# Optimization experiments

Hardware: AMD Instinct MI355X
Metric: run time of the kernel (lower is better)

Reference implementation:

```python
import jax, jax.numpy as jnp
import numpy as np

N_EXPERT = 8
TOP_K = 2
NEG_INF = -1e9  # finite sentinel so softmax grads stay well-defined


def setup_inputs() -> dict:
    key = jax.random.key(0)
    ks = jax.random.split(key, 8)
    B, S, D, F, E = 2, 2048, 1024, 4096, N_EXPERT
    sd = 1.0 / np.sqrt(D)
    sf = 1.0 / np.sqrt(F)
    return {
        "x": jax.random.normal(ks[0], (B, S, D), jnp.float32),
        "noise": jax.random.normal(ks[1], (B, S, E), jnp.float32),
        "Wr": jax.random.normal(ks[2], (D, E), jnp.float32) * sd,
        "br": jnp.zeros((E,), jnp.float32),
        "Wn": jax.random.normal(ks[3], (D, E), jnp.float32) * sd,
        "bn": jnp.zeros((E,), jnp.float32),
        "W1": jax.random.normal(ks[4], (E, D, F), jnp.float32) * sd,
        "b1": jnp.zeros((E, F), jnp.float32),
        "W2": jax.random.normal(ks[5], (E, F, D), jnp.float32) * sf,
        "b2": jnp.zeros((E, D), jnp.float32),
    }


def reference(x, noise, Wr, br, Wn, bn, W1, b1, W2, b2):
    # NoisyTopkRouter: logits + noise * softplus(noise_logits)
    logits = jnp.einsum("bsd,de->bse", x, Wr) + br
    noise_logits = jnp.einsum("bsd,de->bse", x, Wn) + bn
    noisy = logits + noise * jax.nn.softplus(noise_logits)

    # keep only top-k logits, -inf elsewhere, softmax over experts
    _, top_ids = jax.lax.top_k(noisy, TOP_K)                  # [B,S,K]
    sel = jnp.sum(jax.nn.one_hot(top_ids, N_EXPERT, dtype=noisy.dtype), axis=-2) > 0  # [B,S,E]
    gates = jax.nn.softmax(jnp.where(sel, noisy, NEG_INF), axis=-1)  # zeros off top-k

    # Expert MLP: Linear -> ReLU -> Linear (dropout = 0 at inference).
    # Gates are exactly zero for non-selected experts, so the dense einsum
    # combine equals the original masked gather/scatter-add.
    h = jax.nn.relu(jnp.einsum("bsd,edf->ebsf", x, W1) + b1[:, None, None, :])
    eo = jnp.einsum("ebsf,efd->ebsd", h, W2) + b2[:, None, None, :]
    return jnp.einsum("bse,ebsd->bsd", gates, eo)
```

## Files before the change

### kernel.cpp

```cpp
#include <hip/hip_runtime.h>

#define T_TOK 4096
#define DDIM 1024
#define FDIM 4096
#define NE 8
#define NPAIR 8192
#define MAXT128 72
#define MAXT256 48

typedef short bf16x8 __attribute__((ext_vector_type(8)));
typedef float f32x4 __attribute__((ext_vector_type(4)));

__device__ inline unsigned short f2bf(float f) {
  union { float f; unsigned u; } a; a.f = f;
  unsigned r = a.u + 0x7fffu + ((a.u >> 16) & 1u);
  return (unsigned short)(r >> 16);
}

__device__ inline float bf2f(ushort u) {
  union { unsigned u; float f; } a; a.u = ((unsigned)u) << 16;
  return a.f;
}

__device__ __forceinline__ void gload16(const void* g, void* l) {
  __builtin_amdgcn_global_load_lds(
      (const __attribute__((address_space(1))) unsigned int*)g,
      (__attribute__((address_space(3))) unsigned int*)l, 16, 0, 0);
}

__global__ __launch_bounds__(256) void router_kernel(
    const float* __restrict__ x, const float* __restrict__ noise,
    const float* __restrict__ Wr, const float* __restrict__ br,
    const float* __restrict__ Wn, const float* __restrict__ bn,
    int* __restrict__ tok_top, float* __restrict__ tok_gate,
    ushort* __restrict__ xb)
{
  int t = blockIdx.x * 4 + (threadIdx.x >> 6);
  int lane = threadIdx.x & 63;
  const float* xr = x + (size_t)t * DDIM;
  ushort* xo = xb + (size_t)t * DDIM;
  float accR[NE] = {}, accN[NE] = {};
  for (int d = lane; d < DDIM; d += 64) {
    float xv = xr[d];
    xo[d] = f2bf(xv);
    const float* wr = Wr + (size_t)d * NE;
    const float* wn = Wn + (size_t)d * NE;
#pragma unroll
    for (int e = 0; e < NE; ++e) {
      accR[e] = fmaf(xv, wr[e], accR[e]);
      accN[e] = fmaf(xv, wn[e], accN[e]);
    }
  }
#pragma unroll
  for (int off = 32; off > 0; off >>= 1) {
#pragma unroll
    for (int e = 0; e < NE; ++e) {
      accR[e] += __shfl_xor(accR[e], off);
      accN[e] += __shfl_xor(accN[e], off);
    }
  }
  if (lane == 0) {
    float noisy[NE];
#pragma unroll
    for (int e = 0; e < NE; ++e) {
      float lg = accR[e] + br[e];
      float nl = accN[e] + bn[e];
      float sp = fmaxf(nl, 0.f) + log1pf(expf(-fabsf(nl)));
      noisy[e] = lg + noise[(size_t)t * NE + e] * sp;
    }
    int e0 = 0;
#pragma unroll
    for (int e = 1; e < NE; ++e) if (noisy[e] > noisy[e0]) e0 = e;
    int e1 = (e0 == 0) ? 1 : 0;
#pragma unroll
    for (int e = 0; e < NE; ++e)
      if (e != e0 && e != e1 && noisy[e] > noisy[e1]) e1 = e;
    float v0 = noisy[e0], v1 = noisy[e1];
    float ex = __expf(v1 - v0);
    float inv = 1.f / (1.f + ex);
    tok_top[t * 2] = e0; tok_top[t * 2 + 1] = e1;
    tok_gate[t * 2] = inv; tok_gate[t * 2 + 1] = ex * inv;
  }
}

__global__ __launch_bounds__(256) void scan_scatter_kernel(
    const int* __restrict__ tok_top, int* __restrict__ off,
    int* __restrict__ tiles128, int* __restrict__ tiles256,
    int* __restrict__ pair_tok, int* __restrict__ tok_ppos)
{
  __shared__ int smat[NE][256];
  __shared__ int tot[NE];
  __shared__ int loff[NE];
  int tid = threadIdx.x;
  int c[NE] = {};
  for (int i = 0; i < 16; ++i) {
    int t = tid * 16 + i;
    int e0 = tok_top[2 * t], e1 = tok_top[2 * t + 1];
#pragma unroll
    for (int e = 0; e < NE; ++e) c[e] += (e0 == e) + (e1 == e);
  }
#pragma unroll
  for (int e = 0; e < NE; ++e) smat[e][tid] = c[e];
  __syncthreads();
  {
    int ge = tid >> 5;
    int gl = tid & 31;
    int vals[8], s = 0;
#pragma unroll
    for (int j = 0; j < 8; ++j) { vals[j] = smat[ge][gl * 8 + j]; s += vals[j]; }
    int incl = s;
#pragma unroll
    for (int d = 1; d < 32; d <<= 1) {
      int o = __shfl_up(incl, d);
      if (gl >= d) incl += o;
    }
    int run = incl - s;
#pragma unroll
    for (int j = 0; j < 8; ++j) { smat[ge][gl * 8 + j] = run; run += vals[j]; }
    if (gl == 31) tot[ge] = incl;
  }
  __syncthreads();
  if (tid == 0) {
    int s = 0, nt1 = 0, nt2 = 0;
    for (int e = 0; e < NE; ++e) {
      loff[e] = s; off[e] = s;
      int t1 = (tot[e] + 127) >> 7;
      for (int m = 0; m < t1; ++m) tiles128[1 + nt1++] = (e << 8) | m;
      int t2 = (tot[e] + 255) >> 8;
      for (int m = 0; m < t2; ++m) tiles256[1 + nt2++] = (e << 8) | m;
      s += tot[e];
    }
    off[NE] = s;
    tiles128[0] = nt1;
    tiles256[0] = nt2;
  }
  __syncthreads();
  for (int i = 0; i < 16; ++i) {
    int t = tid * 16 + i;
#pragma unroll
    for (int k = 0; k < 2; ++k) {
      int e = tok_top[2 * t + k];
      int pos = loff[e] + smat[e][tid];
      smat[e][tid] = smat[e][tid] + 1;
      pair_tok[pos] = t;
      tok_ppos[2 * t + k] = pos;
    }
  }
}

__global__ __launch_bounds__(256) void transpose_w1_kernel(
    const float* __restrict__ W1, ushort* __restrict__ WT1)
{
  __shared__ float tile[64][65];
  int z = blockIdx.z;
  const float* src = W1 + (size_t)z * DDIM * FDIM;
  ushort* dst = WT1 + (size_t)z * FDIM * DDIM;
  int c0 = blockIdx.x * 64, r0 = blockIdx.y * 64;
  int tid = threadIdx.x;
  int tr = tid >> 4;
  int tc4 = (tid & 15) * 4;
#pragma unroll
  for (int i = 0; i < 64; i += 16) {
    float4 v = *(const float4*)(src + (size_t)(r0 + tr + i) * FDIM + c0 + tc4);
    tile[tr + i][tc4] = v.x; tile[tr + i][tc4 + 1] = v.y;
    tile[tr + i][tc4 + 2] = v.z; tile[tr + i][tc4 + 3] = v.w;
  }
  __syncthreads();
  int rr = (tid & 7) * 8;
  int cbase = tid >> 3;
#pragma unroll
  for (int cc = 0; cc < 64; cc += 32) {
    int c = cbase + cc;
    ushort tmp[8];
#pragma unroll
    for (int j = 0; j < 8; ++j) tmp[j] = f2bf(tile[rr + j][c]);
    *(uint4*)(dst + (size_t)(c0 + c) * DDIM + r0 + rr) = *(uint4*)tmp;
  }
}

template<int KD, int ND, int INDIR>
__global__ __launch_bounds__(512) void gemm8p_kernel(
    const ushort* __restrict__ A, const ushort* __restrict__ BT,
    const int* __restrict__ off, const int* __restrict__ tiles,
    const int* __restrict__ pair_tok, const float* __restrict__ bias,
    ushort* __restrict__ Hout,
    const float* __restrict__ W2src, ushort* __restrict__ WT2dst)
{
  constexpr int GX = ND / 256;
  constexpr int NKT = KD / 64;
  constexpr int NIT = NKT / 2;
  __shared__ __align__(16) char lds[2 * 65536];

  int total = tiles[0] * GX;
  int orig = blockIdx.x + GX * (int)blockIdx.y;
  if (orig >= total) {
    int S = GX * (int)gridDim.y - total;
    int half = threadIdx.x >> 8;
    int tid2 = threadIdx.x & 255;
    float (*tt)[65] = (float(*)[65])(lds + half * 16704);
    int tr = tid2 >> 4, tc4 = (tid2 & 15) * 4;
    int rr = (tid2 & 7) * 8, cbase = tid2 >> 3;
    for (int j = orig - total; j < 4096; j += S) {
      int idx = 2 * j + half;
      int e2 = idx >> 10;
      int rem = idx & 1023;
      int ft = rem >> 4, dt = rem & 15;
      const float* src = W2src + (size_t)e2 * FDIM * DDIM;
      ushort* dst = WT2dst + (size_t)e2 * DDIM * FDIM;
      int r0 = ft * 64, c0 = dt * 64;
#pragma unroll
      for (int i = 0; i < 64; i += 16) {
        float4 v = *(const float4*)(src + (size_t)(r0 + tr + i) * DDIM + c0 + tc4);
        tt[tr + i][tc4] = v.x; tt[tr + i][tc4 + 1] = v.y;
        tt[tr + i][tc4 + 2] = v.z; tt[tr + i][tc4 + 3] = v.w;
      }
      __syncthreads();
#pragma unroll
      for (int cc = 0; cc < 64; cc += 32) {
        int c = cbase + cc;
        ushort tmp[8];
#pragma unroll
        for (int jj = 0; jj < 8; ++jj) tmp[jj] = f2bf(tt[rr + jj][c]);
        *(uint4*)(dst + (size_t)(c0 + c) * FDIM + r0 + rr) = *(uint4*)tmp;
      }
      __syncthreads();
    }
    return;
  }
  int q = total >> 3, r = total & 7, xcd = orig & 7, idx = orig >> 3;
  int wg = (xcd < r ? xcd * (q + 1) : r * (q + 1) + (xcd - r) * q) + idx;
  int ti = wg / GX, bx = wg - ti * GX;

  int te = tiles[1 + ti];
  int e = te >> 8, mt = te & 255;
  int base = off[e];
  int cnt = off[e + 1] - base;
  int m0 = mt << 8, n0 = bx << 8;

  int tid = threadIdx.x, lane = tid & 63, wid = tid >> 6;
  int wr = wid >> 2, wc = wid & 3;
  int lr = lane & 15, hi = lane >> 4;
  int swl = (lane & 7) << 4;
  int wrOff = wr * 16384;
  int wcLow = wc & 1;
  int wcHiOff = (wc >> 1) * 16384;

  const char* aptr[2][2];
  const char* bptr[2][2];
  {
    const char* Ab = (const char*)A;
    const char* Bb = (const char*)(BT + ((size_t)e * ND + n0) * KD);
#pragma unroll
    for (int h = 0; h < 2; ++h)
#pragma unroll
      for (int c = 0; c < 2; ++c) {
        int ch = c * 512 + tid;
        int rl = ch >> 3;
        int sc = ((ch & 7) * 16) ^ ((rl & 7) << 4);
        int mr = m0 + h * 128 + rl; if (mr >= cnt) mr = cnt - 1;
        int ar = INDIR ? pair_tok[base + mr] : base + mr;
        aptr[h][c] = Ab + (size_t)ar * (KD * 2) + sc;
        bptr[h][c] = Bb + (size_t)(h * 128 + rl) * (KD * 2) + sc;
      }
  }

#define SH_A(T, H)                                                        \
  if ((T) < NKT) {                                                        \
    char* d_ = lds + ((T) & 1) * 65536 + (H) * 16384 + tid * 16;          \
    gload16(aptr[H][0] + (T) * 128, d_);                                  \
    gload16(aptr[H][1] + (T) * 128, d_ + 8192);                           \
  }
#define SH_B(T, H)                                                        \
  if ((T) < NKT) {                                                        \
    char* d_ = lds + ((T) & 1) * 65536 + 32768 + (H) * 16384 + tid * 16;  \
    gload16(bptr[H][0] + (T) * 128, d_);                                  \
    gload16(bptr[H][1] + (T) * 128, d_ + 8192);                           \
  }
#define LDA(MH, BUF)                                                      \
  { _Pragma("unroll") for (int mm = 0; mm < 4; ++mm) {                    \
      int rr_ = (MH) * 64 + mm * 16 + lr;                                 \
      _Pragma("unroll") for (int ks = 0; ks < 2; ++ks)                    \
        af[mm][ks] = *(const bf16x8*)((BUF) + wrOff + rr_ * 128 +         \
                                      ((ks * 64 + hi * 16) ^ swl)); } }
#define LDB(NH, BUF, BV)                                                  \
  { _Pragma("unroll") for (int nn = 0; nn < 2; ++nn) {                    \
      int rr_ = wcLow * 64 + (NH) * 32 + nn * 16 + lr;                    \
      _Pragma("unroll") for (int ks = 0; ks < 2; ++ks)                    \
        BV[nn][ks] = *(const bf16x8*)((BUF) + 32768 + wcHiOff + rr_ * 128 + \
                                      ((ks * 64 + hi * 16) ^ swl)); } }
#define MMA(MH, NH, BV)                                                   \
  { _Pragma("unroll") for (int ks = 0; ks < 2; ++ks)                      \
    _Pragma("unroll") for (int mm = 0; mm < 4; ++mm)                      \
    _Pragma("unroll") for (int nn = 0; nn < 2; ++nn)                      \
      acc[(MH) * 4 + mm][(NH) * 2 + nn] =                                 \
        __builtin_amdgcn_mfma_f32_16x16x32_bf16(                          \
          af[mm][ks], BV[nn][ks], acc[(MH) * 4 + mm][(NH) * 2 + nn], 0, 0, 0); }
#define PH_MID                                                            \
  __builtin_amdgcn_sched_barrier(0);                                      \
  __builtin_amdgcn_s_barrier();                                           \
  asm volatile("s_waitcnt lgkmcnt(0)" ::: "memory");                      \
  __builtin_amdgcn_sched_barrier(0);                                      \
  __builtin_amdgcn_s_setprio(1);
#define PH_END                                                            \
  __builtin_amdgcn_s_setprio(0);                                          \
  __builtin_amdgcn_sched_barrier(0);                                      \
  __builtin_amdgcn_s_barrier();

  f32x4 acc[8][4] = {};
  bf16x8 af[4][2], bv0[2][2], bv1[2][2];

  SH_A(0, 0); SH_A(0, 1); SH_B(0, 0); SH_B(0, 1); SH_B(1, 0); SH_B(1, 1);
  asm volatile("s_waitcnt vmcnt(4)" ::: "memory");
  __builtin_amdgcn_sched_barrier(0);
  __builtin_amdgcn_s_barrier();

  const char* buf0 = lds;
  const char* buf1 = lds + 65536;

  for (int it = 0; it < NIT; ++it) {
    int t0 = 2 * it, t1 = t0 + 1;
    LDA(0, buf0); LDB(0, buf0, bv0);
    SH_A(t1, 0);
    PH_MID; MMA(0, 0, bv0); PH_END;
    LDB(1, buf0, bv1);
    SH_A(t1, 1);
    PH_MID; MMA(0, 1, bv1); PH_END;
    LDA(1, buf0);
    SH_B(t0 + 2, 0);
    PH_MID; MMA(1, 1, bv1); PH_END;
    SH_A(t0 + 2, 0);
    PH_MID; MMA(1, 0, bv0);
    __builtin_amdgcn_s_setprio(0);
    if (t0 + 2 < NKT) asm volatile("s_waitcnt vmcnt(4)" ::: "memory");
    else              asm volatile("s_waitcnt vmcnt(0)" ::: "memory");
    __builtin_amdgcn_sched_barrier(0);
    __builtin_amdgcn_s_barrier();
    LDA(0, buf1); LDB(0, buf1, bv0);
    SH_A(t0 + 2, 1);
    PH_MID; MMA(0, 0, bv0); PH_END;
    LDB(1, buf1, bv1);
    SH_B(t0 + 2, 1);
    PH_MID; MMA(0, 1, bv1); PH_END;
    LDA(1, buf1);
    SH_B(t1 + 2, 0);
    PH_MID; MMA(1, 1, bv1); PH_END;
    SH_B(t1 + 2, 1);
    PH_MID; MMA(1, 0, bv0);
    __builtin_amdgcn_s_setprio(0);
    if (t1 + 2 < NKT) asm volatile("s_waitcnt vmcnt(4)" ::: "memory");
    else              asm volatile("s_waitcnt vmcnt(0)" ::: "memory");
    __builtin_amdgcn_sched_barrier(0);
    __builtin_amdgcn_s_barrier();
  }

  int rq = hi << 2;
#pragma unroll
  for (int m = 0; m < 8; ++m) {
#pragma unroll
    for (int qq = 0; qq < 4; ++qq) {
      int rr2 = m0 + wr * 128 + m * 16 + rq + qq;
      if (rr2 < cnt) {
#pragma unroll
        for (int n = 0; n < 4; ++n) {
          int col = n0 + wc * 64 + n * 16 + lr;
          float v = fmaxf(acc[m][n][qq] + bias[(size_t)e * ND + col], 0.f);
          Hout[(size_t)(base + rr2) * ND + col] = f2bf(v);
        }
      }
    }
  }
#undef SH_A
#undef SH_B
#undef LDA
#undef LDB
#undef MMA
#undef PH_MID
#undef PH_END
}

template<int KD, int ND, int EPI, int INDIR>
__global__ __launch_bounds__(256) void gemm4_kernel(
    const ushort* __restrict__ A, const ushort* __restrict__ BT,
    const int* __restrict__ off, const int* __restrict__ tiles,
    const int* __restrict__ pair_tok, const float* __restrict__ bias,
    ushort* __restrict__ Hout, ushort* __restrict__ EOout)
{
  constexpr int GX = ND / 128;
  constexpr int NKT = KD / 64;
  __shared__ __align__(16) ushort As[128 * 64];
  __shared__ __align__(16) ushort Bs[128 * 64];

  int total = tiles[0] * GX;
  int orig = blockIdx.x + GX * (int)blockIdx.y;
  if (orig >= total) return;
  int q = total >> 3, r = total & 7, xcd = orig & 7, idx = orig >> 3;
  int wg = (xcd < r ? xcd * (q + 1) : r * (q + 1) + (xcd - r) * q) + idx;
  int ti = wg / GX, bx = wg - ti * GX;

  int te = tiles[1 + ti];
  int e = te >> 8, mt = te & 255;
  int base = off[e];
  int cnt = off[e + 1] - base;
  int m0 = mt << 7, n0 = bx << 7;

  int tid = threadIdx.x, lane = tid & 63, wid = tid >> 6;
  int wr = wid >> 1, wc = wid & 1;

  int arow[4];
#pragma unroll
  for (int c = 0; c < 4; ++c) {
    int rl = (c * 256 + tid) >> 3;
    int mr = m0 + rl; if (mr >= cnt) mr = cnt - 1;
    arow[c] = INDIR ? pair_tok[base + mr] : base + mr;
  }
  const char* Ab = (const char*)A;
  const char* Bgb = (const char*)(BT + ((size_t)e * ND + n0) * KD);

  f32x4 acc[4][4] = {};

  for (int t = 0; t < NKT; ++t) {
    __syncthreads();
    int kb = t * 128;
#pragma unroll
    for (int c = 0; c < 4; ++c) {
      int ch = c * 256 + tid;
      int row = ch >> 3, b = (ch & 7) * 16;
      gload16(Ab + (size_t)arow[c] * (KD * 2) + kb + (b ^ ((row & 7) << 4)),
              (char*)As + ch * 16);
    }
#pragma unroll
    for (int c = 0; c < 4; ++c) {
      int ch = c * 256 + tid;
      int row = ch >> 3, b = (ch & 7) * 16;
      gload16(Bgb + (size_t)row * (KD * 2) + kb + (b ^ ((row & 7) << 4)),
              (char*)Bs + ch * 16);
    }
    __syncthreads();

    bf16x8 af[4][2], bv[4][2];
#pragma unroll
    for (int m = 0; m < 4; ++m) {
      int row = wr * 64 + m * 16 + (lane & 15);
      int sw = (row & 7) << 4;
#pragma unroll
      for (int ks = 0; ks < 2; ++ks)
        af[m][ks] = *(const bf16x8*)((const char*)As + row * 128 +
                                     ((ks * 64 + (lane >> 4) * 16) ^ sw));
    }
#pragma unroll
    for (int n = 0; n < 4; ++n) {
      int row = wc * 64 + n * 16 + (lane & 15);
      int sw = (row & 7) << 4;
#pragma unroll
      for (int ks = 0; ks < 2; ++ks)
        bv[n][ks] = *(const bf16x8*)((const char*)Bs + row * 128 +
                                     ((ks * 64 + (lane >> 4) * 16) ^ sw));
    }
#pragma unroll
    for (int ks = 0; ks < 2; ++ks)
#pragma unroll
      for (int m = 0; m < 4; ++m)
#pragma unroll
        for (int n = 0; n < 4; ++n)
          acc[m][n] = __builtin_amdgcn_mfma_f32_16x16x32_bf16(
              af[m][ks], bv[n][ks], acc[m][n], 0, 0, 0);
  }

  float bvv[4];
#pragma unroll
  for (int n = 0; n < 4; ++n)
    bvv[n] = bias[(size_t)e * ND + n0 + wc * 64 + n * 16 + (lane & 15)];
  int rq = (lane >> 4) << 2;
#pragma unroll
  for (int m = 0; m < 4; ++m) {
#pragma unroll
    for (int qq = 0; qq < 4; ++qq) {
      int rr = m0 + wr * 64 + m * 16 + rq + qq;
      if (rr < cnt) {
#pragma unroll
        for (int n = 0; n < 4; ++n) {
          int col = n0 + wc * 64 + n * 16 + (lane & 15);
          float v = acc[m][n][qq] + bvv[n];
          if (EPI == 0) v = fmaxf(v, 0.f);
          ushort* dstp = (EPI == 0) ? Hout : EOout;
          dstp[(size_t)(base + rr) * ND + col] = f2bf(v);
        }
      }
    }
  }
}

__global__ __launch_bounds__(256) void combine_kernel(
    const ushort* __restrict__ eo, const int* __restrict__ tok_ppos,
    const float* __restrict__ tok_gate, float* __restrict__ out)
{
  int t = blockIdx.x;
  int tid = threadIdx.x;
  int p0 = tok_ppos[t * 2], p1 = tok_ppos[t * 2 + 1];
  float g0 = tok_gate[t * 2], g1 = tok_gate[t * 2 + 1];
  ushort4 a = ((const ushort4*)(eo + (size_t)p0 * DDIM))[tid];
  ushort4 b = ((const ushort4*)(eo + (size_t)p1 * DDIM))[tid];
  float4 o;
  o.x = g0 * bf2f(a.x) + g1 * bf2f(b.x);
  o.y = g0 * bf2f(a.y) + g1 * bf2f(b.y);
  o.z = g0 * bf2f(a.z) + g1 * bf2f(b.z);
  o.w = g0 * bf2f(a.w) + g1 * bf2f(b.w);
  ((float4*)(out + (size_t)t * DDIM))[tid] = o;
}

extern "C" void kernel_launch(void* const* d_in, const int* in_sizes, int n_in,
                              void* d_out, int out_size, void* d_ws, size_t ws_size,
                              hipStream_t stream)
{
  const float* x     = (const float*)d_in[0];
  const float* noise = (const float*)d_in[1];
  const float* Wr    = (const float*)d_in[2];
  const float* br    = (const float*)d_in[3];
  const float* Wn    = (const float*)d_in[4];
  const float* bn    = (const float*)d_in[5];
  const float* W1    = (const float*)d_in[6];
  const float* b1    = (const float*)d_in[7];
  const float* W2    = (const float*)d_in[8];
  const float* b2    = (const float*)d_in[9];
  float* out = (float*)d_out;

  char* ws = (char*)d_ws;
  size_t o = 0;
  auto alloc = [&](size_t sz) {
    void* p = ws + o;
    o = (o + sz + 255) & ~(size_t)255;
    return p;
  };
  ushort* WT1 = (ushort*)alloc((size_t)NE * FDIM * DDIM * 2);
  ushort* WT2 = (ushort*)alloc((size_t)NE * DDIM * FDIM * 2);
  ushort* XB  = (ushort*)alloc((size_t)T_TOK * DDIM * 2);
  ushort* H   = (ushort*)alloc((size_t)(NPAIR + 256) * FDIM * 2);
  ushort* EO  = (ushort*)alloc((size_t)(NPAIR + 256) * DDIM * 2);
  int*    TOK_TOP  = (int*)alloc(T_TOK * 2 * 4);
  float*  TOK_GATE = (float*)alloc(T_TOK * 2 * 4);
  int*    TOK_PPOS = (int*)alloc(T_TOK * 2 * 4);
  int*    PAIR_TOK = (int*)alloc((NPAIR + 256) * 4);
  int*    OFF = (int*)alloc(64);
  int*    TILES128 = (int*)alloc((1 + MAXT128) * 4);
  int*    TILES256 = (int*)alloc((1 + MAXT256) * 4);

  router_kernel<<<T_TOK / 4, 256, 0, stream>>>(x, noise, Wr, br, Wn, bn,
                                               TOK_TOP, TOK_GATE, XB);
  scan_scatter_kernel<<<1, 256, 0, stream>>>(TOK_TOP, OFF, TILES128, TILES256,
                                             PAIR_TOK, TOK_PPOS);
  transpose_w1_kernel<<<dim3(64, 16, 8), 256, 0, stream>>>(W1, WT1);
  gemm8p_kernel<DDIM, FDIM, 1>
      <<<dim3(FDIM / 256, MAXT256), 512, 0, stream>>>(XB, WT1, OFF, TILES256, PAIR_TOK,
                                                      b1, H, W2, WT2);
  gemm4_kernel<FDIM, DDIM, 1, 0>
      <<<dim3(DDIM / 128, MAXT128), 256, 0, stream>>>(H, WT2, OFF, TILES128, PAIR_TOK,
                                                      b2, nullptr, EO);
  combine_kernel<<<T_TOK, 256, 0, stream>>>(EO, TOK_PPOS, TOK_GATE, out);
}
```

Before: 310.6 us.

## Replace second expert GEMM with double-buffered, interleaved-prefetch pipelined kernel

```diff
diff --git a/kernel.cpp b/kernel.cpp
--- a/kernel.cpp
+++ b/kernel.cpp
@@ -374,21 +374,18 @@
 #undef LDA
 #undef LDB
 #undef MMA
-#undef PH_MID
-#undef PH_END
-}
-
-template<int KD, int ND, int EPI, int INDIR>
-__global__ __launch_bounds__(256) void gemm4_kernel(
+}
+
+template<int KD, int ND>
+__global__ __launch_bounds__(256) void gemm8p2_kernel(
     const ushort* __restrict__ A, const ushort* __restrict__ BT,
     const int* __restrict__ off, const int* __restrict__ tiles,
-    const int* __restrict__ pair_tok, const float* __restrict__ bias,
-    ushort* __restrict__ Hout, ushort* __restrict__ EOout)
+    const float* __restrict__ bias, ushort* __restrict__ EOout)
 {
   constexpr int GX = ND / 128;
   constexpr int NKT = KD / 64;
-  __shared__ __align__(16) ushort As[128 * 64];
-  __shared__ __align__(16) ushort Bs[128 * 64];
+  constexpr int NIT = NKT / 2;
+  __shared__ __align__(16) char lds[2 * 32768];
 
   int total = tiles[0] * GX;
   int orig = blockIdx.x + GX * (int)blockIdx.y;
@@ -405,89 +402,131 @@
 
   int tid = threadIdx.x, lane = tid & 63, wid = tid >> 6;
   int wr = wid >> 1, wc = wid & 1;
-
-  int arow[4];
-#pragma unroll
-  for (int c = 0; c < 4; ++c) {
-    int rl = (c * 256 + tid) >> 3;
-    int mr = m0 + rl; if (mr >= cnt) mr = cnt - 1;
-    arow[c] = INDIR ? pair_tok[base + mr] : base + mr;
-  }
-  const char* Ab = (const char*)A;
-  const char* Bgb = (const char*)(BT + ((size_t)e * ND + n0) * KD);
+  int lr = lane & 15, hi = lane >> 4;
+  int swl = (lane & 7) << 4;
+  int wrOff = wr * 8192;
+  int wcOff = 16384 + wc * 8192;
+
+  const char* aptr[2][2];
+  const char* bptr[2][2];
+  {
+    const char* Ab = (const char*)A;
+    const char* Bb = (const char*)(BT + ((size_t)e * ND + n0) * KD);
+#pragma unroll
+    for (int h = 0; h < 2; ++h)
+#pragma unroll
+      for (int c = 0; c < 2; ++c) {
+        int ch = c * 256 + tid;
+        int rl = ch >> 3;
+        int sc = ((ch & 7) * 16) ^ ((rl & 7) << 4);
+        int mr = m0 + h * 64 + rl; if (mr >= cnt) mr = cnt - 1;
+        aptr[h][c] = Ab + (size_t)(base + mr) * (KD * 2) + sc;
+        bptr[h][c] = Bb + (size_t)(h * 64 + rl) * (KD * 2) + sc;
+      }
+  }
+
+#define SH_A(T, H)                                                        \
+  if ((T) < NKT) {                                                        \
+    char* d_ = lds + ((T) & 1) * 32768 + (H) * 8192 + tid * 16;           \
+    gload16(aptr[H][0] + (T) * 128, d_);                                  \
+    gload16(aptr[H][1] + (T) * 128, d_ + 4096);                           \
+  }
+#define SH_B(T, H)                                                        \
+  if ((T) < NKT) {                                                        \
+    char* d_ = lds + ((T) & 1) * 32768 + 16384 + (H) * 8192 + tid * 16;   \
+    gload16(bptr[H][0] + (T) * 128, d_);                                  \
+    gload16(bptr[H][1] + (T) * 128, d_ + 4096);                           \
+  }
+#define LDA(MH, BUF)                                                      \
+  { _Pragma("unroll") for (int mm = 0; mm < 2; ++mm) {                    \
+      int rr_ = (MH) * 32 + mm * 16 + lr;                                 \
+      _Pragma("unroll") for (int ks = 0; ks < 2; ++ks)                    \
+        af[mm][ks] = *(const bf16x8*)((BUF) + wrOff + rr_ * 128 +         \
+                                      ((ks * 64 + hi * 16) ^ swl)); } }
+#define LDB(NH, BUF, BV)                                                  \
+  { _Pragma("unroll") for (int nn = 0; nn < 2; ++nn) {                    \
+      int rr_ = (NH) * 32 + nn * 16 + lr;                                 \
+      _Pragma("unroll") for (int ks = 0; ks < 2; ++ks)                    \
+        BV[nn][ks] = *(const bf16x8*)((BUF) + wcOff + rr_ * 128 +         \
+                                      ((ks * 64 + hi * 16) ^ swl)); } }
+#define MMA(MH, NH, BV)                                                   \
+  { _Pragma("unroll") for (int ks = 0; ks < 2; ++ks)                      \
+    _Pragma("unroll") for (int mm = 0; mm < 2; ++mm)                      \
+    _Pragma("unroll") for (int nn = 0; nn < 2; ++nn)                      \
+      acc[(MH) * 2 + mm][(NH) * 2 + nn] =                                 \
+        __builtin_amdgcn_mfma_f32_16x16x32_bf16(                          \
+          af[mm][ks], BV[nn][ks], acc[(MH) * 2 + mm][(NH) * 2 + nn], 0, 0, 0); }
 
   f32x4 acc[4][4] = {};
-
-  for (int t = 0; t < NKT; ++t) {
-    __syncthreads();
-    int kb = t * 128;
-#pragma unroll
-    for (int c = 0; c < 4; ++c) {
-      int ch = c * 256 + tid;
-      int row = ch >> 3, b = (ch & 7) * 16;
-      gload16(Ab + (size_t)arow[c] * (KD * 2) + kb + (b ^ ((row & 7) << 4)),
-              (char*)As + ch * 16);
-    }
-#pragma unroll
-    for (int c = 0; c < 4; ++c) {
-      int ch = c * 256 + tid;
-      int row = ch >> 3, b = (ch & 7) * 16;
-      gload16(Bgb + (size_t)row * (KD * 2) + kb + (b ^ ((row & 7) << 4)),
-              (char*)Bs + ch * 16);
-    }
-    __syncthreads();
-
-    bf16x8 af[4][2], bv[4][2];
-#pragma unroll
-    for (int m = 0; m < 4; ++m) {
-      int row = wr * 64 + m * 16 + (lane & 15);
-      int sw = (row & 7) << 4;
-#pragma unroll
-      for (int ks = 0; ks < 2; ++ks)
-        af[m][ks] = *(const bf16x8*)((const char*)As + row * 128 +
-                                     ((ks * 64 + (lane >> 4) * 16) ^ sw));
-    }
-#pragma unroll
-    for (int n = 0; n < 4; ++n) {
-      int row = wc * 64 + n * 16 + (lane & 15);
-      int sw = (row & 7) << 4;
-#pragma unroll
-      for (int ks = 0; ks < 2; ++ks)
-        bv[n][ks] = *(const bf16x8*)((const char*)Bs + row * 128 +
-                                     ((ks * 64 + (lane >> 4) * 16) ^ sw));
-    }
-#pragma unroll
-    for (int ks = 0; ks < 2; ++ks)
-#pragma unroll
-      for (int m = 0; m < 4; ++m)
-#pragma unroll
-        for (int n = 0; n < 4; ++n)
-          acc[m][n] = __builtin_amdgcn_mfma_f32_16x16x32_bf16(
-              af[m][ks], bv[n][ks], acc[m][n], 0, 0, 0);
-  }
-
-  float bvv[4];
-#pragma unroll
-  for (int n = 0; n < 4; ++n)
-    bvv[n] = bias[(size_t)e * ND + n0 + wc * 64 + n * 16 + (lane & 15)];
-  int rq = (lane >> 4) << 2;
+  bf16x8 af[2][2], bv0[2][2], bv1[2][2];
+
+  SH_A(0, 0); SH_A(0, 1); SH_B(0, 0); SH_B(0, 1); SH_B(1, 0); SH_B(1, 1);
+  asm volatile("s_waitcnt vmcnt(4)" ::: "memory");
+  __builtin_amdgcn_sched_barrier(0);
+  __builtin_amdgcn_s_barrier();
+
+  const char* buf0 = lds;
+  const char* buf1 = lds + 32768;
+
+  for (int it = 0; it < NIT; ++it) {
+    int t0 = 2 * it, t1 = t0 + 1;
+    LDA(0, buf0); LDB(0, buf0, bv0);
+    SH_A(t1, 0);
+    PH_MID; MMA(0, 0, bv0); PH_END;
+    LDB(1, buf0, bv1);
+    SH_A(t1, 1);
+    PH_MID; MMA(0, 1, bv1); PH_END;
+    LDA(1, buf0);
+    SH_B(t0 + 2, 0);
+    PH_MID; MMA(1, 1, bv1); PH_END;
+    SH_A(t0 + 2, 0);
+    PH_MID; MMA(1, 0, bv0);
+    __builtin_amdgcn_s_setprio(0);
+    if (t0 + 2 < NKT) asm volatile("s_waitcnt vmcnt(4)" ::: "memory");
+    else              asm volatile("s_waitcnt vmcnt(0)" ::: "memory");
+    __builtin_amdgcn_sched_barrier(0);
+    __builtin_amdgcn_s_barrier();
+    LDA(0, buf1); LDB(0, buf1, bv0);
+    SH_A(t0 + 2, 1);
+    PH_MID; MMA(0, 0, bv0); PH_END;
+    LDB(1, buf1, bv1);
+    SH_B(t0 + 2, 1);
+    PH_MID; MMA(0, 1, bv1); PH_END;
+    LDA(1, buf1);
+    SH_B(t1 + 2, 0);
+    PH_MID; MMA(1, 1, bv1); PH_END;
+    SH_B(t1 + 2, 1);
+    PH_MID; MMA(1, 0, bv0);
+    __builtin_amdgcn_s_setprio(0);
+    if (t1 + 2 < NKT) asm volatile("s_waitcnt vmcnt(4)" ::: "memory");
+    else              asm volatile("s_waitcnt vmcnt(0)" ::: "memory");
+    __builtin_amdgcn_sched_barrier(0);
+    __builtin_amdgcn_s_barrier();
+  }
+
+  int rq = hi << 2;
 #pragma unroll
   for (int m = 0; m < 4; ++m) {
 #pragma unroll
     for (int qq = 0; qq < 4; ++qq) {
-      int rr = m0 + wr * 64 + m * 16 + rq + qq;
-      if (rr < cnt) {
+      int rr2 = m0 + wr * 64 + m * 16 + rq + qq;
+      if (rr2 < cnt) {
 #pragma unroll
         for (int n = 0; n < 4; ++n) {
-          int col = n0 + wc * 64 + n * 16 + (lane & 15);
-          float v = acc[m][n][qq] + bvv[n];
-          if (EPI == 0) v = fmaxf(v, 0.f);
-          ushort* dstp = (EPI == 0) ? Hout : EOout;
-          dstp[(size_t)(base + rr) * ND + col] = f2bf(v);
+          int col = n0 + wc * 64 + n * 16 + lr;
+          float v = acc[m][n][qq] + bias[(size_t)e * ND + col];
+          EOout[(size_t)(base + rr2) * ND + col] = f2bf(v);
         }
       }
     }
   }
+#undef SH_A
+#undef SH_B
+#undef LDA
+#undef LDB
+#undef MMA
+#undef PH_MID
+#undef PH_END
 }
 
 __global__ __launch_bounds__(256) void combine_kernel(
@@ -552,8 +591,7 @@
   gemm8p_kernel<DDIM, FDIM, 1>
       <<<dim3(FDIM / 256, MAXT256), 512, 0, stream>>>(XB, WT1, OFF, TILES256, PAIR_TOK,
                                                       b1, H, W2, WT2);
-  gemm4_kernel<FDIM, DDIM, 1, 0>
-      <<<dim3(DDIM / 128, MAXT128), 256, 0, stream>>>(H, WT2, OFF, TILES128, PAIR_TOK,
-                                                      b2, nullptr, EO);
+  gemm8p2_kernel<FDIM, DDIM>
+      <<<dim3(DDIM / 128, MAXT128), 256, 0, stream>>>(H, WT2, OFF, TILES128, b2, EO);
   combine_kernel<<<T_TOK, 256, 0, stream>>>(EO, TOK_PPOS, TOK_GATE, out);
 }
```

After: 319.6 us. 2.9% more time.
